# Kernel optimization log

Measured on AMD Instinct MI355X. Metric: run time of the kernel, lower is better.

Reference implementation:

```python
import jax, jax.numpy as jnp
import numpy as np

B, C, H, W = 4, 128, 64, 64
NUM_HEADS = 4
HEAD_DIM = C // NUM_HEADS


def setup_inputs() -> dict:
    key = jax.random.key(0)
    ks = jax.random.split(key, 9)
    s = 0.02
    return {
        "x": jax.random.normal(ks[0], (B, C, H, W), dtype=jnp.float32),
        "wq": jax.random.normal(ks[1], (C, C), dtype=jnp.float32) * s,
        "bq": jax.random.normal(ks[2], (C,), dtype=jnp.float32) * s,
        "wk": jax.random.normal(ks[3], (C, C), dtype=jnp.float32) * s,
        "bk": jax.random.normal(ks[4], (C,), dtype=jnp.float32) * s,
        "wv": jax.random.normal(ks[5], (C, C), dtype=jnp.float32) * s,
        "bv": jax.random.normal(ks[6], (C,), dtype=jnp.float32) * s,
        "wo": jax.random.normal(ks[7], (C, C), dtype=jnp.float32) * s,
        "bo": jax.random.normal(ks[8], (C,), dtype=jnp.float32) * s,
    }


def _proj(w, b, xf):
    # 1x1 conv == channel-mixing linear: xf is (B, C, N)
    return jnp.einsum("oc,bcn->bon", w, xf) + b[None, :, None]


def reference(x, wq, bq, wk, bk, wv, bv, wo, bo):
    b, c, h, w = x.shape
    n = h * w
    nh, hd = NUM_HEADS, HEAD_DIM
    xf = x.reshape(b, c, n)
    q = _proj(wq, bq, xf).reshape(b, nh, hd, n)
    k = _proj(wk, bk, xf).reshape(b, nh, hd, n)
    v = _proj(wv, bv, xf).reshape(b, nh, hd, n)
    # scores: (b, heads, n, n)
    scores = jnp.einsum("bhdn,bhdm->bhnm", q, k) / jnp.sqrt(jnp.float32(hd)).astype(x.dtype)
    prob = jax.nn.softmax(scores, axis=-1)
    # attn_out: (b, heads, head_dim, n)
    attn = jnp.einsum("bhnm,bhdm->bhdn", prob, v).reshape(b, c, n)
    out = _proj(wo, bo, attn).reshape(b, c, h, w)
    return x + out
```

## Files before the change

### kernel.cpp

```cpp
#include <hip/hip_runtime.h>
#include <hip/hip_bf16.h>

#define BB 4
#define CC 128
#define NN 4096
#define NHEAD 4
#define HDIM 32
#define KSPLIT 2

typedef short bf16x8_t __attribute__((ext_vector_type(8)));
typedef float f32x4_t __attribute__((ext_vector_type(4)));
typedef int i32x4_t __attribute__((ext_vector_type(4)));

#define MFMA16(a, b, c) __builtin_amdgcn_mfma_f32_16x16x32_bf16(a, b, c, 0, 0, 0)
#define EXP2(x) __builtin_amdgcn_exp2f(x)

#define QSCALE (0.17677669529663687f * 1.4426950408889634f)

static __device__ inline unsigned short f2bf(float f) {
  unsigned u = __builtin_bit_cast(unsigned, f);
  u += 0x7fffu + ((u >> 16) & 1u);
  return (unsigned short)(u >> 16);
}
static __device__ inline unsigned pk2(float lo, float hi) {
  return (unsigned)f2bf(lo) | ((unsigned)f2bf(hi) << 16);
}
static __device__ inline unsigned pack_trunc(float lo, float hi) {
  return __builtin_amdgcn_perm(__builtin_bit_cast(unsigned, hi),
                               __builtin_bit_cast(unsigned, lo), 0x07060302u);
}

static __device__ inline void gload_lds16(const unsigned short* gsrc, void* ldst) {
  __builtin_amdgcn_global_load_lds(
      (const __attribute__((address_space(1))) unsigned int*)gsrc,
      (__attribute__((address_space(3))) unsigned int*)ldst, 16, 0, 0);
}

__global__ __launch_bounds__(256) void wconv_kernel(
    const float* __restrict__ wq, const float* __restrict__ wk,
    const float* __restrict__ wv, const float* __restrict__ wo,
    unsigned short* __restrict__ wb) {
  int f = (blockIdx.x * 256 + threadIdx.x) * 8;
  int m = f >> 14, off = f & 16383;
  const float* src = (m == 0) ? wq : (m == 1) ? wk : (m == 2) ? wv : wo;
  float sc = (m == 0) ? QSCALE : 1.0f;
  float4 a = *(const float4*)(src + off);
  float4 b = *(const float4*)(src + off + 4);
  ushort4 u0, u1;
  u0.x = f2bf(a.x * sc); u0.y = f2bf(a.y * sc); u0.z = f2bf(a.z * sc); u0.w = f2bf(a.w * sc);
  u1.x = f2bf(b.x * sc); u1.y = f2bf(b.y * sc); u1.z = f2bf(b.z * sc); u1.w = f2bf(b.w * sc);
  *(ushort4*)(wb + f) = u0;
  *(ushort4*)(wb + f + 4) = u1;
}

__global__ __launch_bounds__(256) void xconv_kernel(
    const float* __restrict__ x, unsigned short* __restrict__ xbT) {
  __shared__ __attribute__((aligned(16))) unsigned short xs[64][136];
  const int b = blockIdx.y, nt = blockIdx.x;
  const int tid = threadIdx.x;
#pragma unroll
  for (int i = 0; i < 8; i++) {
    int f = tid + 256 * i;
    int c = f >> 4, n4 = (f & 15) * 4;
    float4 v4 = *(const float4*)(x + ((size_t)b * CC + c) * NN + nt * 64 + n4);
    xs[n4 + 0][c] = f2bf(v4.x);
    xs[n4 + 1][c] = f2bf(v4.y);
    xs[n4 + 2][c] = f2bf(v4.z);
    xs[n4 + 3][c] = f2bf(v4.w);
  }
  __syncthreads();
  unsigned short* dst = xbT + ((size_t)b * NN + nt * 64) * CC;
#pragma unroll
  for (int i = 0; i < 4; i++) {
    int f = tid + 256 * i;
    int n = f >> 4, c0 = (f & 15) * 8;
    *(uint4*)(dst + f * 8) = *(const uint4*)&xs[n][c0];
  }
}

__global__ __launch_bounds__(256) void qkv_mfma_kernel(
    const unsigned short* __restrict__ xbT,
    const unsigned short* __restrict__ wqb, const unsigned short* __restrict__ wkb,
    const unsigned short* __restrict__ wvb,
    const float* __restrict__ bq, const float* __restrict__ bk,
    const float* __restrict__ bv,
    unsigned short* __restrict__ qt, unsigned short* __restrict__ kt,
    unsigned short* __restrict__ vg) {
  __shared__ unsigned short vt[128][66];
  const int b = blockIdx.y, nt = blockIdx.x, proj = blockIdx.z;
  const int tid = threadIdx.x;
  const int lane = tid & 63, w = tid >> 6;
  const int l16 = lane & 15, g = lane >> 4;
  const int nl = w * 16;
  const int ngl = nt * 64 + nl;

  const unsigned short* xrow = xbT + ((size_t)b * NN + ngl + l16) * CC + g * 8;
  bf16x8_t xf[4];
#pragma unroll
  for (int ks = 0; ks < 4; ks++)
    xf[ks] = *(const bf16x8_t*)(xrow + ks * 32);

  const unsigned short* wm = (proj == 0) ? wqb : (proj == 1) ? wkb : wvb;
  const float* bias = (proj == 0) ? bq : (proj == 1) ? bk : bv;
  const float bsc = (proj == 0) ? QSCALE : 1.0f;
  unsigned short* qkdst = proj ? kt : qt;

#pragma unroll
  for (int ot = 0; ot < 8; ot++) {
    f32x4_t acc;
#pragma unroll
    for (int r = 0; r < 4; r++) acc[r] = bias[ot * 16 + g * 4 + r] * bsc;
#pragma unroll
    for (int ks = 0; ks < 4; ks++) {
      bf16x8_t wf = *(const bf16x8_t*)(wm + (size_t)(ot * 16 + l16) * CC + ks * 32 + g * 8);
      acc = MFMA16(wf, xf[ks], acc);
    }
    if (proj < 2) {
      unsigned p0 = pk2(acc[0], acc[1]);
      unsigned p1 = pk2(acc[2], acc[3]);
      unsigned q0 = (unsigned)__shfl_xor((int)p0, 16);
      unsigned q1 = (unsigned)__shfl_xor((int)p1, 16);
      if ((g & 1) == 0) {
        int hh = ot >> 1, dblk = (ot & 1) * 2 + (g >> 1);
        unsigned short* dst =
            qkdst + (((size_t)(b * NHEAD + hh) * 4 + dblk) * NN + ngl + l16) * 8;
        uint4 val = make_uint4(p0, p1, q0, q1);
        *(uint4*)dst = val;
      }
    } else {
#pragma unroll
      for (int r = 0; r < 4; r++) vt[ot * 16 + g * 4 + r][nl + l16] = f2bf(acc[r]);
    }
  }

  if (proj == 2) {
    __syncthreads();
#pragma unroll
    for (int c = 0; c < 4; c++) {
      int cid = c * 256 + tid;
      int hh = cid >> 8, inner = cid & 255;
      int g2 = inner & 3, l16v = (inner >> 2) & 15, fh = inner >> 6;
      int fv = fh >> 1, half = fh & 1;
      int o = hh * 32 + half * 16 + l16v;
      int n0 = fv * 32 + g2 * 4;
      unsigned d0 = *(const unsigned*)&vt[o][n0];
      unsigned d1 = *(const unsigned*)&vt[o][n0 + 2];
      unsigned d2 = *(const unsigned*)&vt[o][n0 + 16];
      unsigned d3 = *(const unsigned*)&vt[o][n0 + 18];
      uint4 val = make_uint4(d0, d1, d2, d3);
      *(uint4*)(vg + (((size_t)(b * NHEAD + hh) * 64 + nt) * 256 + inner) * 8) = val;
    }
  }
}

__global__ __launch_bounds__(256, 4) void attn_mfma5_kernel(
    const unsigned short* __restrict__ qt, const unsigned short* __restrict__ kt,
    const unsigned short* __restrict__ vg,
    float* __restrict__ opart, float* __restrict__ lpart) {
  __shared__ __attribute__((aligned(16))) unsigned short smem[2][4096];

  const int chunk = blockIdx.x & (KSPLIT - 1), nt = blockIdx.x / KSPLIT;
  const int h = blockIdx.y, b = blockIdx.z;
  const int bh = b * NHEAD + h;
  const int tid = threadIdx.x, lane = tid & 63, wid = tid >> 6;
  const int l16 = lane & 15, g = lane >> 4;
  const int nbase = nt * 128 + wid * 32;

  const unsigned short* qb = qt + (size_t)bh * NN * HDIM;
  const unsigned short* kb = kt + (size_t)bh * NN * HDIM;
  const unsigned short* vgb = vg + (size_t)bh * 64 * 2048;

  const bf16x8_t qf0 = *(const bf16x8_t*)(qb + ((size_t)g * NN + nbase + l16) * 8);
  const bf16x8_t qf1 = *(const bf16x8_t*)(qb + ((size_t)g * NN + nbase + 16 + l16) * 8);

  f32x4_t o00 = {0, 0, 0, 0}, o01 = {0, 0, 0, 0};
  f32x4_t o10 = {0, 0, 0, 0}, o11 = {0, 0, 0, 0};
  f32x4_t la = {0, 0, 0, 0}, lb = {0, 0, 0, 0};
  const f32x4_t zf = {0, 0, 0, 0};
  const i32x4_t onesi = {0x3F803F80, 0x3F803F80, 0x3F803F80, 0x3F803F80};
  const bf16x8_t ones = __builtin_bit_cast(bf16x8_t, onesi);

  const int NITER = 64 / KSPLIT;
  const int mt0 = chunk * NITER;

  const unsigned short* ksrc = kb + ((size_t)g * NN + mt0 * 64 + wid * 16 + l16) * 8;
  const unsigned short* vsrc = vgb + (size_t)mt0 * 2048 + (size_t)((wid * 16 + l16) * 4 + g) * 8;

  auto stage = [&](int p, int i) {
    gload_lds16(ksrc + (size_t)i * 512, &smem[p][wid * 512]);
    gload_lds16(vsrc + (size_t)i * 2048, &smem[p][2048 + wid * 512]);
  };

  auto body = [&](int p) {
    const unsigned short* sk = &smem[p][0];
    bf16x8_t k0 = *(const bf16x8_t*)(sk + 0 * 512 + lane * 8);
    bf16x8_t k1 = *(const bf16x8_t*)(sk + 1 * 512 + lane * 8);
    bf16x8_t k2 = *(const bf16x8_t*)(sk + 2 * 512 + lane * 8);
    bf16x8_t k3 = *(const bf16x8_t*)(sk + 3 * 512 + lane * 8);
    bf16x8_t vf0 = *(const bf16x8_t*)(sk + 2048 + 0 * 512 + lane * 8);
    bf16x8_t vf2 = *(const bf16x8_t*)(sk + 2048 + 1 * 512 + lane * 8);
    bf16x8_t vf1 = *(const bf16x8_t*)(sk + 2048 + 2 * 512 + lane * 8);
    bf16x8_t vf3 = *(const bf16x8_t*)(sk + 2048 + 3 * 512 + lane * 8);

    f32x4_t sA0 = MFMA16(k0, qf0, zf), sA1 = MFMA16(k1, qf0, zf);
    f32x4_t sA2 = MFMA16(k2, qf0, zf), sA3 = MFMA16(k3, qf0, zf);
    f32x4_t sB0 = MFMA16(k0, qf1, zf), sB1 = MFMA16(k1, qf1, zf);
    f32x4_t sB2 = MFMA16(k2, qf1, zf), sB3 = MFMA16(k3, qf1, zf);

#pragma unroll
    for (int r = 0; r < 4; r++) {
      sA0[r] = EXP2(sA0[r]); sA1[r] = EXP2(sA1[r]);
      sA2[r] = EXP2(sA2[r]); sA3[r] = EXP2(sA3[r]);
      sB0[r] = EXP2(sB0[r]); sB1[r] = EXP2(sB1[r]);
      sB2[r] = EXP2(sB2[r]); sB3[r] = EXP2(sB3[r]);
    }

    i32x4_t pA0i = {(int)pack_trunc(sA0[0], sA0[1]), (int)pack_trunc(sA0[2], sA0[3]),
                    (int)pack_trunc(sA1[0], sA1[1]), (int)pack_trunc(sA1[2], sA1[3])};
    i32x4_t pA1i = {(int)pack_trunc(sA2[0], sA2[1]), (int)pack_trunc(sA2[2], sA2[3]),
                    (int)pack_trunc(sA3[0], sA3[1]), (int)pack_trunc(sA3[2], sA3[3])};
    i32x4_t pB0i = {(int)pack_trunc(sB0[0], sB0[1]), (int)pack_trunc(sB0[2], sB0[3]),
                    (int)pack_trunc(sB1[0], sB1[1]), (int)pack_trunc(sB1[2], sB1[3])};
    i32x4_t pB1i = {(int)pack_trunc(sB2[0], sB2[1]), (int)pack_trunc(sB2[2], sB2[3]),
                    (int)pack_trunc(sB3[0], sB3[1]), (int)pack_trunc(sB3[2], sB3[3])};
    bf16x8_t pA0 = __builtin_bit_cast(bf16x8_t, pA0i);
    bf16x8_t pA1 = __builtin_bit_cast(bf16x8_t, pA1i);
    bf16x8_t pB0 = __builtin_bit_cast(bf16x8_t, pB0i);
    bf16x8_t pB1 = __builtin_bit_cast(bf16x8_t, pB1i);

    o00 = MFMA16(vf0, pA0, o00); o00 = MFMA16(vf1, pA1, o00);
    o01 = MFMA16(vf2, pA0, o01); o01 = MFMA16(vf3, pA1, o01);
    o10 = MFMA16(vf0, pB0, o10); o10 = MFMA16(vf1, pB1, o10);
    o11 = MFMA16(vf2, pB0, o11); o11 = MFMA16(vf3, pB1, o11);

    la = MFMA16(ones, pA0, la); la = MFMA16(ones, pA1, la);
    lb = MFMA16(ones, pB0, lb); lb = MFMA16(ones, pB1, lb);
  };

  stage(0, 0);
  __syncthreads();
  for (int mi = 0; mi < NITER; mi += 2) {
    stage(1, mi + 1);
    body(0);
    __syncthreads();
    if (mi + 2 < NITER) stage(0, mi + 2);
    body(1);
    __syncthreads();
  }

  float* obase = opart + ((size_t)(chunk * BB * NHEAD + bh)) * HDIM * NN;
#pragma unroll
  for (int r = 0; r < 4; r++) {
    obase[(size_t)(g * 4 + r) * NN + nbase + l16] = o00[r];
    obase[(size_t)(16 + g * 4 + r) * NN + nbase + l16] = o01[r];
    obase[(size_t)(g * 4 + r) * NN + nbase + 16 + l16] = o10[r];
    obase[(size_t)(16 + g * 4 + r) * NN + nbase + 16 + l16] = o11[r];
  }
  if (g == 0) {
    float* lb_ = lpart + (size_t)(chunk * BB * NHEAD + bh) * NN;
    lb_[nbase + l16] = la[0];
    lb_[nbase + 16 + l16] = lb[0];
  }
}

__global__ __launch_bounds__(512) void out_mfma_kernel(
    const float* __restrict__ opart, const float* __restrict__ lpart,
    const unsigned short* __restrict__ wob, const float* __restrict__ bo,
    const float* __restrict__ x, float* __restrict__ out) {
  __shared__ __attribute__((aligned(16))) unsigned short xsb[64][136];
  __shared__ float linv[NHEAD][64];
  const int b = blockIdx.y, nt = blockIdx.x;
  const int tid = threadIdx.x;

  if (tid < 256) {
    int h = tid >> 6, nn = tid & 63;
    int bh = b * NHEAD + h;
    float l = 0.f;
#pragma unroll
    for (int c = 0; c < KSPLIT; c++)
      l += lpart[(size_t)(c * BB * NHEAD + bh) * NN + nt * 64 + nn];
    linv[h][nn] = 1.f / l;
  }
  __syncthreads();

  const float* ob = opart + (size_t)b * NHEAD * HDIM * NN;
  const size_t CH = (size_t)BB * NHEAD * HDIM * NN;
#pragma unroll
  for (int i = 0; i < 4; i++) {
    int s = i * 512 + tid;
    int cd = s >> 4, n4 = (s & 15) * 4;
    size_t a = (size_t)cd * NN + nt * 64 + n4;
    float4 v0 = *(const float4*)(ob + a);
    float4 v1 = *(const float4*)(ob + CH + a);
    const float* li = &linv[cd >> 5][n4];
    xsb[n4 + 0][cd] = f2bf((v0.x + v1.x) * li[0]);
    xsb[n4 + 1][cd] = f2bf((v0.y + v1.y) * li[1]);
    xsb[n4 + 2][cd] = f2bf((v0.z + v1.z) * li[2]);
    xsb[n4 + 3][cd] = f2bf((v0.w + v1.w) * li[3]);
  }
  __syncthreads();

  const int lane = tid & 63, w = tid >> 6;
  const int l16 = lane & 15, g = lane >> 4;
  const int nsub = (w & 3) * 16, mtbase = (w >> 2) * 4;
  const int n0 = nt * 64 + nsub;

  bf16x8_t bfr[4];
#pragma unroll
  for (int ks = 0; ks < 4; ks++)
    bfr[ks] = *(const bf16x8_t*)&xsb[nsub + l16][ks * 32 + g * 8];

#pragma unroll
  for (int mi = 0; mi < 4; mi++) {
    int mt = mtbase + mi;
    f32x4_t acc;
#pragma unroll
    for (int r = 0; r < 4; r++) acc[r] = bo[mt * 16 + g * 4 + r];
#pragma unroll
    for (int ks = 0; ks < 4; ks++) {
      bf16x8_t af = *(const bf16x8_t*)(wob + (size_t)(mt * 16 + l16) * CC + ks * 32 + g * 8);
      acc = MFMA16(af, bfr[ks], acc);
    }
#pragma unroll
    for (int r = 0; r < 4; r++) {
      int o = mt * 16 + g * 4 + r;
      size_t addr = ((size_t)b * CC + o) * NN + n0 + l16;
      out[addr] = acc[r] + x[addr];
    }
  }
}

extern "C" void kernel_launch(void* const* d_in, const int* in_sizes, int n_in,
                              void* d_out, int out_size, void* d_ws, size_t ws_size,
                              hipStream_t stream) {
  const float* x  = (const float*)d_in[0];
  const float* wq = (const float*)d_in[1];
  const float* bq = (const float*)d_in[2];
  const float* wk = (const float*)d_in[3];
  const float* bk = (const float*)d_in[4];
  const float* wv = (const float*)d_in[5];
  const float* bv = (const float*)d_in[6];
  const float* wo = (const float*)d_in[7];
  const float* bo = (const float*)d_in[8];
  float* out = (float*)d_out;

  char* w = (char*)d_ws;
  const size_t SZ = (size_t)BB * NHEAD * NN * HDIM * 2;
  unsigned short* qt    = (unsigned short*)w;
  unsigned short* kt    = (unsigned short*)(w + SZ);
  unsigned short* vg    = (unsigned short*)(w + 2 * SZ);
  unsigned short* wb    = (unsigned short*)(w + 3 * SZ);
  float* opart = (float*)(w + 3 * SZ + 131072);
  float* lpart = (float*)(w + 3 * SZ + 131072 +
                          (size_t)KSPLIT * BB * NHEAD * HDIM * NN * 4);
  unsigned short* xbT = (unsigned short*)opart;
  unsigned short* wqb = wb, *wkb = wb + 16384, *wvb = wb + 32768, *wob = wb + 49152;

  wconv_kernel<<<32, 256, 0, stream>>>(wq, wk, wv, wo, wb);
  xconv_kernel<<<dim3(NN / 64, BB), 256, 0, stream>>>(x, xbT);
  qkv_mfma_kernel<<<dim3(NN / 64, BB, 3), 256, 0, stream>>>(
      xbT, wqb, wkb, wvb, bq, bk, bv, qt, kt, vg);
  attn_mfma5_kernel<<<dim3((NN / 128) * KSPLIT, NHEAD, BB), 256, 0, stream>>>(
      qt, kt, vg, opart, lpart);
  out_mfma_kernel<<<dim3(NN / 64, BB), 512, 0, stream>>>(
      opart, lpart, wob, bo, x, out);
}
```

Baseline: 145.1 us.

## Split attention keys four ways, store partials in bf16, raise MFMA priority

Doubles the key-dimension split of the attention kernel to four chunks and raises the occupancy hint to 8 blocks per CU. This puts more blocks on the GPU and shortens each block's serial loop. The unnormalized partial outputs are now written as bf16 instead of fp32, halving partial-output traffic, and the output kernel sums all four chunks. MFMA sections are wrapped in s_setprio to favour matrix issue across waves. The bf16 partials add rounding error before the reduction, and the larger split adds more partial reads in the output kernel.

```diff
diff --git a/kernel.cpp b/kernel.cpp
--- a/kernel.cpp
+++ b/kernel.cpp
@@ -6,7 +6,7 @@
 #define NN 4096
 #define NHEAD 4
 #define HDIM 32
-#define KSPLIT 2
+#define KSPLIT 4
 
 typedef short bf16x8_t __attribute__((ext_vector_type(8)));
 typedef float f32x4_t __attribute__((ext_vector_type(4)));
@@ -21,6 +21,9 @@
   unsigned u = __builtin_bit_cast(unsigned, f);
   u += 0x7fffu + ((u >> 16) & 1u);
   return (unsigned short)(u >> 16);
+}
+static __device__ inline float bf2f(unsigned short u) {
+  return __builtin_bit_cast(float, (unsigned)u << 16);
 }
 static __device__ inline unsigned pk2(float lo, float hi) {
   return (unsigned)f2bf(lo) | ((unsigned)f2bf(hi) << 16);
@@ -153,10 +156,10 @@
   }
 }
 
-__global__ __launch_bounds__(256, 4) void attn_mfma5_kernel(
+__global__ __launch_bounds__(256, 8) void attn_mfma5_kernel(
     const unsigned short* __restrict__ qt, const unsigned short* __restrict__ kt,
     const unsigned short* __restrict__ vg,
-    float* __restrict__ opart, float* __restrict__ lpart) {
+    unsigned short* __restrict__ opart, float* __restrict__ lpart) {
   __shared__ __attribute__((aligned(16))) unsigned short smem[2][4096];
 
   const int chunk = blockIdx.x & (KSPLIT - 1), nt = blockIdx.x / KSPLIT;
@@ -202,10 +205,12 @@
     bf16x8_t vf1 = *(const bf16x8_t*)(sk + 2048 + 2 * 512 + lane * 8);
     bf16x8_t vf3 = *(const bf16x8_t*)(sk + 2048 + 3 * 512 + lane * 8);
 
+    __builtin_amdgcn_s_setprio(1);
     f32x4_t sA0 = MFMA16(k0, qf0, zf), sA1 = MFMA16(k1, qf0, zf);
     f32x4_t sA2 = MFMA16(k2, qf0, zf), sA3 = MFMA16(k3, qf0, zf);
     f32x4_t sB0 = MFMA16(k0, qf1, zf), sB1 = MFMA16(k1, qf1, zf);
     f32x4_t sB2 = MFMA16(k2, qf1, zf), sB3 = MFMA16(k3, qf1, zf);
+    __builtin_amdgcn_s_setprio(0);
 
 #pragma unroll
     for (int r = 0; r < 4; r++) {
@@ -228,6 +233,7 @@
     bf16x8_t pB0 = __builtin_bit_cast(bf16x8_t, pB0i);
     bf16x8_t pB1 = __builtin_bit_cast(bf16x8_t, pB1i);
 
+    __builtin_amdgcn_s_setprio(1);
     o00 = MFMA16(vf0, pA0, o00); o00 = MFMA16(vf1, pA1, o00);
     o01 = MFMA16(vf2, pA0, o01); o01 = MFMA16(vf3, pA1, o01);
     o10 = MFMA16(vf0, pB0, o10); o10 = MFMA16(vf1, pB1, o10);
@@ -235,6 +241,7 @@
 
     la = MFMA16(ones, pA0, la); la = MFMA16(ones, pA1, la);
     lb = MFMA16(ones, pB0, lb); lb = MFMA16(ones, pB1, lb);
+    __builtin_amdgcn_s_setprio(0);
   };
 
   stage(0, 0);
@@ -248,13 +255,13 @@
     __syncthreads();
   }
 
-  float* obase = opart + ((size_t)(chunk * BB * NHEAD + bh)) * HDIM * NN;
+  unsigned short* obase = opart + ((size_t)(chunk * BB * NHEAD + bh)) * HDIM * NN;
 #pragma unroll
   for (int r = 0; r < 4; r++) {
-    obase[(size_t)(g * 4 + r) * NN + nbase + l16] = o00[r];
-    obase[(size_t)(16 + g * 4 + r) * NN + nbase + l16] = o01[r];
-    obase[(size_t)(g * 4 + r) * NN + nbase + 16 + l16] = o10[r];
-    obase[(size_t)(16 + g * 4 + r) * NN + nbase + 16 + l16] = o11[r];
+    obase[(size_t)(g * 4 + r) * NN + nbase + l16] = f2bf(o00[r]);
+    obase[(size_t)(16 + g * 4 + r) * NN + nbase + l16] = f2bf(o01[r]);
+    obase[(size_t)(g * 4 + r) * NN + nbase + 16 + l16] = f2bf(o10[r]);
+    obase[(size_t)(16 + g * 4 + r) * NN + nbase + 16 + l16] = f2bf(o11[r]);
   }
   if (g == 0) {
     float* lb_ = lpart + (size_t)(chunk * BB * NHEAD + bh) * NN;
@@ -264,7 +271,7 @@
 }
 
 __global__ __launch_bounds__(512) void out_mfma_kernel(
-    const float* __restrict__ opart, const float* __restrict__ lpart,
+    const unsigned short* __restrict__ opart, const float* __restrict__ lpart,
     const unsigned short* __restrict__ wob, const float* __restrict__ bo,
     const float* __restrict__ x, float* __restrict__ out) {
   __shared__ __attribute__((aligned(16))) unsigned short xsb[64][136];
@@ -283,20 +290,24 @@
   }
   __syncthreads();
 
-  const float* ob = opart + (size_t)b * NHEAD * HDIM * NN;
+  const unsigned short* ob = opart + (size_t)b * NHEAD * HDIM * NN;
   const size_t CH = (size_t)BB * NHEAD * HDIM * NN;
 #pragma unroll
   for (int i = 0; i < 4; i++) {
     int s = i * 512 + tid;
     int cd = s >> 4, n4 = (s & 15) * 4;
     size_t a = (size_t)cd * NN + nt * 64 + n4;
-    float4 v0 = *(const float4*)(ob + a);
-    float4 v1 = *(const float4*)(ob + CH + a);
+    float s0 = 0.f, s1 = 0.f, s2 = 0.f, s3 = 0.f;
+#pragma unroll
+    for (int c = 0; c < KSPLIT; c++) {
+      ushort4 u = *(const ushort4*)(ob + c * CH + a);
+      s0 += bf2f(u.x); s1 += bf2f(u.y); s2 += bf2f(u.z); s3 += bf2f(u.w);
+    }
     const float* li = &linv[cd >> 5][n4];
-    xsb[n4 + 0][cd] = f2bf((v0.x + v1.x) * li[0]);
-    xsb[n4 + 1][cd] = f2bf((v0.y + v1.y) * li[1]);
-    xsb[n4 + 2][cd] = f2bf((v0.z + v1.z) * li[2]);
-    xsb[n4 + 3][cd] = f2bf((v0.w + v1.w) * li[3]);
+    xsb[n4 + 0][cd] = f2bf(s0 * li[0]);
+    xsb[n4 + 1][cd] = f2bf(s1 * li[1]);
+    xsb[n4 + 2][cd] = f2bf(s2 * li[2]);
+    xsb[n4 + 3][cd] = f2bf(s3 * li[3]);
   }
   __syncthreads();
 
@@ -350,10 +361,10 @@
   unsigned short* kt    = (unsigned short*)(w + SZ);
   unsigned short* vg    = (unsigned short*)(w + 2 * SZ);
   unsigned short* wb    = (unsigned short*)(w + 3 * SZ);
-  float* opart = (float*)(w + 3 * SZ + 131072);
+  unsigned short* opart = (unsigned short*)(w + 3 * SZ + 131072);
   float* lpart = (float*)(w + 3 * SZ + 131072 +
-                          (size_t)KSPLIT * BB * NHEAD * HDIM * NN * 4);
-  unsigned short* xbT = (unsigned short*)opart;
+                          (size_t)KSPLIT * BB * NHEAD * HDIM * NN * 2);
+  unsigned short* xbT = opart;
   unsigned short* wqb = wb, *wkb = wb + 16384, *wvb = wb + 32768, *wob = wb + 49152;
 
   wconv_kernel<<<32, 256, 0, stream>>>(wq, wk, wv, wo, wb);
```

Measured after the change: 368.4 us. 154% more time.

## Fuse weight and input bf16 conversion into projection kernels; raise MFMA priority

Applied to the files above, without the earlier changes.

Removes the separate weight-conversion and x-transpose kernels. Each projection block now loads the fp32 weights and its x tile, converts them to bf16 in LDS, and reads MFMA operands from LDS. The out-projection kernel converts wo the same way. This saves two kernel launches and the xbT global round trip, at the cost of every block redundantly converting a full 128x128 weight matrix. s_setprio is also wrapped around the MFMA groups in the attention loop to favour matrix issue over the other waves.

```diff
diff --git a/kernel.cpp b/kernel.cpp
--- a/kernel.cpp
+++ b/kernel.cpp
@@ -36,71 +36,58 @@
       (__attribute__((address_space(3))) unsigned int*)ldst, 16, 0, 0);
 }
 
-__global__ __launch_bounds__(256) void wconv_kernel(
+__global__ __launch_bounds__(256) void qkv_mfma_kernel(
+    const float* __restrict__ x,
     const float* __restrict__ wq, const float* __restrict__ wk,
-    const float* __restrict__ wv, const float* __restrict__ wo,
-    unsigned short* __restrict__ wb) {
-  int f = (blockIdx.x * 256 + threadIdx.x) * 8;
-  int m = f >> 14, off = f & 16383;
-  const float* src = (m == 0) ? wq : (m == 1) ? wk : (m == 2) ? wv : wo;
-  float sc = (m == 0) ? QSCALE : 1.0f;
-  float4 a = *(const float4*)(src + off);
-  float4 b = *(const float4*)(src + off + 4);
-  ushort4 u0, u1;
-  u0.x = f2bf(a.x * sc); u0.y = f2bf(a.y * sc); u0.z = f2bf(a.z * sc); u0.w = f2bf(a.w * sc);
-  u1.x = f2bf(b.x * sc); u1.y = f2bf(b.y * sc); u1.z = f2bf(b.z * sc); u1.w = f2bf(b.w * sc);
-  *(ushort4*)(wb + f) = u0;
-  *(ushort4*)(wb + f + 4) = u1;
-}
-
-__global__ __launch_bounds__(256) void xconv_kernel(
-    const float* __restrict__ x, unsigned short* __restrict__ xbT) {
-  __shared__ __attribute__((aligned(16))) unsigned short xs[64][136];
-  const int b = blockIdx.y, nt = blockIdx.x;
+    const float* __restrict__ wv,
+    const float* __restrict__ bq, const float* __restrict__ bk,
+    const float* __restrict__ bv,
+    unsigned short* __restrict__ qt, unsigned short* __restrict__ kt,
+    unsigned short* __restrict__ vg) {
+  __shared__ __attribute__((aligned(16))) unsigned short wsb[128][136];
+  __shared__ __attribute__((aligned(16))) unsigned short xsb[64][136];
+  unsigned short(*vt)[66] = (unsigned short(*)[66]) & xsb[0][0];
+
+  const int b = blockIdx.y, nt = blockIdx.x, proj = blockIdx.z;
   const int tid = threadIdx.x;
+
+  const float* wsrc = (proj == 0) ? wq : (proj == 1) ? wk : wv;
+  const float wscale = (proj == 0) ? QSCALE : 1.0f;
+
+#pragma unroll
+  for (int i = 0; i < 16; i++) {
+    int idx = i * 256 + tid;
+    int o = idx >> 5, c4 = (idx & 31) * 4;
+    float4 v4 = *(const float4*)(wsrc + (size_t)o * CC + c4);
+    wsb[o][c4 + 0] = f2bf(v4.x * wscale);
+    wsb[o][c4 + 1] = f2bf(v4.y * wscale);
+    wsb[o][c4 + 2] = f2bf(v4.z * wscale);
+    wsb[o][c4 + 3] = f2bf(v4.w * wscale);
+  }
+
 #pragma unroll
   for (int i = 0; i < 8; i++) {
     int f = tid + 256 * i;
     int c = f >> 4, n4 = (f & 15) * 4;
     float4 v4 = *(const float4*)(x + ((size_t)b * CC + c) * NN + nt * 64 + n4);
-    xs[n4 + 0][c] = f2bf(v4.x);
-    xs[n4 + 1][c] = f2bf(v4.y);
-    xs[n4 + 2][c] = f2bf(v4.z);
-    xs[n4 + 3][c] = f2bf(v4.w);
-  }
-  __syncthreads();
-  unsigned short* dst = xbT + ((size_t)b * NN + nt * 64) * CC;
-#pragma unroll
-  for (int i = 0; i < 4; i++) {
-    int f = tid + 256 * i;
-    int n = f >> 4, c0 = (f & 15) * 8;
-    *(uint4*)(dst + f * 8) = *(const uint4*)&xs[n][c0];
-  }
-}
-
-__global__ __launch_bounds__(256) void qkv_mfma_kernel(
-    const unsigned short* __restrict__ xbT,
-    const unsigned short* __restrict__ wqb, const unsigned short* __restrict__ wkb,
-    const unsigned short* __restrict__ wvb,
-    const float* __restrict__ bq, const float* __restrict__ bk,
-    const float* __restrict__ bv,
-    unsigned short* __restrict__ qt, unsigned short* __restrict__ kt,
-    unsigned short* __restrict__ vg) {
-  __shared__ unsigned short vt[128][66];
-  const int b = blockIdx.y, nt = blockIdx.x, proj = blockIdx.z;
-  const int tid = threadIdx.x;
+    xsb[n4 + 0][c] = f2bf(v4.x);
+    xsb[n4 + 1][c] = f2bf(v4.y);
+    xsb[n4 + 2][c] = f2bf(v4.z);
+    xsb[n4 + 3][c] = f2bf(v4.w);
+  }
+  __syncthreads();
+
   const int lane = tid & 63, w = tid >> 6;
   const int l16 = lane & 15, g = lane >> 4;
   const int nl = w * 16;
   const int ngl = nt * 64 + nl;
 
-  const unsigned short* xrow = xbT + ((size_t)b * NN + ngl + l16) * CC + g * 8;
   bf16x8_t xf[4];
 #pragma unroll
   for (int ks = 0; ks < 4; ks++)
-    xf[ks] = *(const bf16x8_t*)(xrow + ks * 32);
-
-  const unsigned short* wm = (proj == 0) ? wqb : (proj == 1) ? wkb : wvb;
+    xf[ks] = *(const bf16x8_t*)&xsb[nl + l16][ks * 32 + g * 8];
+  __syncthreads();
+
   const float* bias = (proj == 0) ? bq : (proj == 1) ? bk : bv;
   const float bsc = (proj == 0) ? QSCALE : 1.0f;
   unsigned short* qkdst = proj ? kt : qt;
@@ -112,7 +99,7 @@
     for (int r = 0; r < 4; r++) acc[r] = bias[ot * 16 + g * 4 + r] * bsc;
 #pragma unroll
     for (int ks = 0; ks < 4; ks++) {
-      bf16x8_t wf = *(const bf16x8_t*)(wm + (size_t)(ot * 16 + l16) * CC + ks * 32 + g * 8);
+      bf16x8_t wf = *(const bf16x8_t*)&wsb[ot * 16 + l16][ks * 32 + g * 8];
       acc = MFMA16(wf, xf[ks], acc);
     }
     if (proj < 2) {
@@ -202,10 +189,12 @@
     bf16x8_t vf1 = *(const bf16x8_t*)(sk + 2048 + 2 * 512 + lane * 8);
     bf16x8_t vf3 = *(const bf16x8_t*)(sk + 2048 + 3 * 512 + lane * 8);
 
+    __builtin_amdgcn_s_setprio(1);
     f32x4_t sA0 = MFMA16(k0, qf0, zf), sA1 = MFMA16(k1, qf0, zf);
     f32x4_t sA2 = MFMA16(k2, qf0, zf), sA3 = MFMA16(k3, qf0, zf);
     f32x4_t sB0 = MFMA16(k0, qf1, zf), sB1 = MFMA16(k1, qf1, zf);
     f32x4_t sB2 = MFMA16(k2, qf1, zf), sB3 = MFMA16(k3, qf1, zf);
+    __builtin_amdgcn_s_setprio(0);
 
 #pragma unroll
     for (int r = 0; r < 4; r++) {
@@ -228,6 +217,7 @@
     bf16x8_t pB0 = __builtin_bit_cast(bf16x8_t, pB0i);
     bf16x8_t pB1 = __builtin_bit_cast(bf16x8_t, pB1i);
 
+    __builtin_amdgcn_s_setprio(1);
     o00 = MFMA16(vf0, pA0, o00); o00 = MFMA16(vf1, pA1, o00);
     o01 = MFMA16(vf2, pA0, o01); o01 = MFMA16(vf3, pA1, o01);
     o10 = MFMA16(vf0, pB0, o10); o10 = MFMA16(vf1, pB1, o10);
@@ -235,6 +225,7 @@
 
     la = MFMA16(ones, pA0, la); la = MFMA16(ones, pA1, la);
     lb = MFMA16(ones, pB0, lb); lb = MFMA16(ones, pB1, lb);
+    __builtin_amdgcn_s_setprio(0);
   };
 
   stage(0, 0);
@@ -265,12 +256,24 @@
 
 __global__ __launch_bounds__(512) void out_mfma_kernel(
     const float* __restrict__ opart, const float* __restrict__ lpart,
-    const unsigned short* __restrict__ wob, const float* __restrict__ bo,
+    const float* __restrict__ wo, const float* __restrict__ bo,
     const float* __restrict__ x, float* __restrict__ out) {
+  __shared__ __attribute__((aligned(16))) unsigned short wsb[128][136];
   __shared__ __attribute__((aligned(16))) unsigned short xsb[64][136];
   __shared__ float linv[NHEAD][64];
   const int b = blockIdx.y, nt = blockIdx.x;
   const int tid = threadIdx.x;
+
+#pragma unroll
+  for (int i = 0; i < 8; i++) {
+    int idx = i * 512 + tid;
+    int o = idx >> 5, c4 = (idx & 31) * 4;
+    float4 v4 = *(const float4*)(wo + (size_t)o * CC + c4);
+    wsb[o][c4 + 0] = f2bf(v4.x);
+    wsb[o][c4 + 1] = f2bf(v4.y);
+    wsb[o][c4 + 2] = f2bf(v4.z);
+    wsb[o][c4 + 3] = f2bf(v4.w);
+  }
 
   if (tid < 256) {
     int h = tid >> 6, nn = tid & 63;
@@ -318,7 +321,7 @@
     for (int r = 0; r < 4; r++) acc[r] = bo[mt * 16 + g * 4 + r];
 #pragma unroll
     for (int ks = 0; ks < 4; ks++) {
-      bf16x8_t af = *(const bf16x8_t*)(wob + (size_t)(mt * 16 + l16) * CC + ks * 32 + g * 8);
+      bf16x8_t af = *(const bf16x8_t*)&wsb[mt * 16 + l16][ks * 32 + g * 8];
       acc = MFMA16(af, bfr[ks], acc);
     }
 #pragma unroll
@@ -349,19 +352,14 @@
   unsigned short* qt    = (unsigned short*)w;
   unsigned short* kt    = (unsigned short*)(w + SZ);
   unsigned short* vg    = (unsigned short*)(w + 2 * SZ);
-  unsigned short* wb    = (unsigned short*)(w + 3 * SZ);
-  float* opart = (float*)(w + 3 * SZ + 131072);
-  float* lpart = (float*)(w + 3 * SZ + 131072 +
+  float* opart = (float*)(w + 3 * SZ);
+  float* lpart = (float*)(w + 3 * SZ +
                           (size_t)KSPLIT * BB * NHEAD * HDIM * NN * 4);
-  unsigned short* xbT = (unsigned short*)opart;
-  unsigned short* wqb = wb, *wkb = wb + 16384, *wvb = wb + 32768, *wob = wb + 49152;
-
-  wconv_kernel<<<32, 256, 0, stream>>>(wq, wk, wv, wo, wb);
-  xconv_kernel<<<dim3(NN / 64, BB), 256, 0, stream>>>(x, xbT);
+
   qkv_mfma_kernel<<<dim3(NN / 64, BB, 3), 256, 0, stream>>>(
-      xbT, wqb, wkb, wvb, bq, bk, bv, qt, kt, vg);
+      x, wq, wk, wv, bq, bk, bv, qt, kt, vg);
   attn_mfma5_kernel<<<dim3((NN / 128) * KSPLIT, NHEAD, BB), 256, 0, stream>>>(
       qt, kt, vg, opart, lpart);
   out_mfma_kernel<<<dim3(NN / 64, BB), 512, 0, stream>>>(
-      opart, lpart, wob, bo, x, out);
-}
+      opart, lpart, wo, bo, x, out);
+}
```

Result: faster. 132.7 us (-8.5%).
